# Optimization experiments

Hardware: AMD Instinct MI355X
Metric: run time of the kernel (lower is better)

Reference implementation:

```python
import jax, jax.numpy as jnp
import numpy as np

B, T, D = 2, 4096, 1024
H, HD = 16, 64
KV = H * HD  # 1024


def setup_inputs() -> dict:
    key = jax.random.key(0)
    ks = jax.random.split(key, 6)
    sc = lambda k, shape, s: jax.random.normal(k, shape, jnp.float32) * s
    return {
        "x": sc(ks[0], (B, T, D), 1.0),
        "W_in": sc(ks[1], (D, 4 * KV), D ** -0.5),      # in_proj (in, out) layout
        "W_ba": sc(ks[2], (D, 2 * H), D ** -0.5),       # ba_proj
        "conv_w": sc(ks[3], (3 * KV, 1, 4), 0.5),       # depthwise conv, (O, I/groups=1, K)
        "dt_bias": jnp.ones((H,), jnp.float32),
        "A_log": jnp.log(jax.random.uniform(ks[4], (H,), jnp.float32, 1e-3, 16.0)),
        "norm_w": jnp.ones((HD,), jnp.float32),
        "W_o": sc(ks[5], (KV, D), KV ** -0.5),
    }


def _l2norm(t, eps=1e-6):
    return t * jax.lax.rsqrt(jnp.sum(t * t, axis=-1, keepdims=True) + eps)


def reference(x, W_in, W_ba, conv_w, dt_bias, A_log, norm_w, W_o):
    Bb, Tt, _ = x.shape
    qkvz = x @ W_in                                  # [B,T,4*KV]
    q, k, v, z = jnp.split(qkvz, 4, axis=-1)
    b, a = jnp.split(x @ W_ba, 2, axis=-1)           # [B,T,H] each

    # causal depthwise conv (kernel 4, left pad 3) + SiLU on concat(q,k,v)
    qkv = jnp.concatenate([q, k, v], axis=-1).transpose(0, 2, 1)  # [B,3KV,T]
    qkv = jax.lax.conv_general_dilated(
        qkv, conv_w, window_strides=(1,), padding=[(3, 0)],
        feature_group_count=3 * KV, dimension_numbers=("NCH", "OIH", "NCH"))
    qkv = jax.nn.silu(qkv).transpose(0, 2, 1)        # [B,T,3KV]
    q, k, v = jnp.split(qkv, 3, axis=-1)

    rs = lambda t: t.reshape(Bb, Tt, H, HD)
    q, k, v, z = rs(q), rs(k), rs(v), rs(z)

    beta = jax.nn.sigmoid(b)                         # [B,T,H]
    A = jnp.exp(jnp.maximum(A_log, -2.3))            # [H]
    g = -A * jax.nn.softplus(a + dt_bias)            # [B,T,H], log decay <= 0

    # fla use_qk_l2norm_in_kernel=True: l2-normalize q,k; q scaled by d^-0.5
    q = _l2norm(q) * (HD ** -0.5)
    k = _l2norm(k)

    # gated delta rule recurrence over time (state S: [B,H,dk,dv])
    tm = lambda t: jnp.swapaxes(t, 0, 1)             # time-major

    def step(S, inp):
        qt, kt, vt, gt, bt = inp
        S = S * jnp.exp(gt)[..., None, None]
        pred = jnp.einsum("bhk,bhkv->bhv", kt, S)
        S = S + jnp.einsum("bhk,bhv->bhkv", kt, (vt - pred) * bt[..., None])
        o = jnp.einsum("bhk,bhkv->bhv", qt, S)
        return S, o

    S0 = jnp.zeros((Bb, H, HD, HD), jnp.float32)
    _, y = jax.lax.scan(step, S0, (tm(q), tm(k), tm(v), tm(g), tm(beta)))
    y = jnp.swapaxes(y, 0, 1)                        # [B,T,H,HD]

    # RMSNormGated over head_dim, gated by silu(z)
    y = y * jax.lax.rsqrt(jnp.mean(y * y, axis=-1, keepdims=True) + 1e-6)
    y = (norm_w * y) * jax.nn.silu(z)

    return y.reshape(Bb, Tt, KV) @ W_o
```

## Files before the change

kernel.cpp:

```cpp
#include <hip/hip_runtime.h>

typedef unsigned short u16;
typedef unsigned int u32;
typedef __attribute__((ext_vector_type(8))) __bf16 bf16x8;
typedef __attribute__((ext_vector_type(8))) _Float16 f16x8;
typedef __attribute__((ext_vector_type(4))) _Float16 f16x4;
typedef __attribute__((ext_vector_type(4))) float f32x4;

#define DEV __device__ __forceinline__

DEV u16 f2bf(float f) {
  u32 u = __float_as_uint(f);
  u += 0x7FFFu + ((u >> 16) & 1u);
  return (u16)(u >> 16);
}
DEV float bf2f(u16 h) { return __uint_as_float(((u32)h) << 16); }
DEV void splitbf(float f, u16& hi, u16& lo) {
  u16 h = f2bf(f);
  hi = h;
  lo = f2bf(f - bf2f(h));
}
DEV void split4(float4 v, ushort4& hh, ushort4& ll) {
  splitbf(v.x, hh.x, ll.x);
  splitbf(v.y, hh.y, ll.y);
  splitbf(v.z, hh.z, ll.z);
  splitbf(v.w, hh.w, ll.w);
}
DEV int SW(int r, int c) { return r * 64 + ((c) ^ ((r & 7) << 3)); }

#define MFMA16(a,b,c) __builtin_amdgcn_mfma_f32_16x16x32_bf16((a),(b),(c),0,0,0)
#define MFMAH(a,b,c)  __builtin_amdgcn_mfma_f32_16x16x32_f16((a),(b),(c),0,0,0)
#define GLDS16(g,l) __builtin_amdgcn_global_load_lds((__attribute__((address_space(1))) void*)(g), (__attribute__((address_space(3))) void*)(l), 16, 0, 0)

DEV f32x4 mm3(bf16x8 ah, bf16x8 al, bf16x8 bh, bf16x8 bl, f32x4 acc) {
  acc = MFMA16(ah, bl, acc);
  acc = MFMA16(al, bh, acc);
  acc = MFMA16(ah, bh, acc);
  return acc;
}

__global__ __launch_bounds__(256) void k_cast_h(const float* __restrict__ in, _Float16* __restrict__ out, int n) {
  int idx = (blockIdx.x * 256 + threadIdx.x) * 4;
  if (idx + 3 < n) {
    float4 v = *(const float4*)(in + idx);
    f16x4 o = {(_Float16)v.x, (_Float16)v.y, (_Float16)v.z, (_Float16)v.w};
    *(f16x4*)(out + idx) = o;
  }
}

__global__ __launch_bounds__(256) void k_transpose_h(const float* __restrict__ in, _Float16* __restrict__ out, int R, int Cc) {
  __shared__ float tile[64][65];
  int c0 = blockIdx.x * 64, r0 = blockIdx.y * 64;
  int lr = threadIdx.x >> 6, lc = threadIdx.x & 63;
#pragma unroll
  for (int i = 0; i < 16; ++i) {
    int r = lr + i * 4;
    tile[r][lc] = in[(size_t)(r0 + r) * Cc + c0 + lc];
  }
  __syncthreads();
#pragma unroll
  for (int i = 0; i < 16; ++i) {
    int oc = lr + i * 4;
    out[(size_t)(c0 + oc) * R + r0 + lc] = (_Float16)tile[lc][oc];
  }
}

__global__ __launch_bounds__(256) void k_transpose(const float* __restrict__ in, u16* __restrict__ out, int R, int Cc) {
  __shared__ float tile[64][65];
  int c0 = blockIdx.x * 64, r0 = blockIdx.y * 64;
  int lr = threadIdx.x >> 6, lc = threadIdx.x & 63;
#pragma unroll
  for (int i = 0; i < 16; ++i) {
    int r = lr + i * 4;
    tile[r][lc] = in[(size_t)(r0 + r) * Cc + c0 + lc];
  }
  __syncthreads();
#pragma unroll
  for (int i = 0; i < 16; ++i) {
    int oc = lr + i * 4;
    out[(size_t)(c0 + oc) * R + r0 + lc] = f2bf(tile[lc][oc]);
  }
}

__global__ __launch_bounds__(256) void k_gemm_h(const _Float16* __restrict__ A, const _Float16* __restrict__ Bt,
                                                u16* __restrict__ Cq, u16* __restrict__ Cz, int M, int N, int K) {
  __shared__ __align__(16) u16 As[128 * 32];
  __shared__ __align__(16) u16 Bs[128 * 32];
  const int tid = threadIdx.x;
  const int nwg = gridDim.x * gridDim.y;
  int bid = blockIdx.y * gridDim.x + blockIdx.x;
  bid = (bid & 7) * (nwg >> 3) + (bid >> 3);
  const int m0 = (bid / gridDim.x) * 128, n0 = (bid % gridDim.x) * 128;
  const int w = tid >> 6, l = tid & 63;
  const int wr = (w >> 1) * 64, wc = (w & 1) * 64;
  const int lrow = l & 15, lk = (l >> 4) * 8, rbase = (l >> 4) * 4;
  const int srow = tid >> 2, scol = (tid & 3) * 8;

  f32x4 acc[4][4];
#pragma unroll
  for (int i = 0; i < 4; ++i)
#pragma unroll
    for (int j = 0; j < 4; ++j) acc[i][j] = {0.f, 0.f, 0.f, 0.f};

  const _Float16* aBase = A + (size_t)m0 * K;
  const _Float16* bBase = Bt + (size_t)n0 * K;

  for (int k0 = 0; k0 < K; k0 += 32) {
    __syncthreads();
    GLDS16(aBase + (size_t)srow * K + k0 + scol,        &As[tid * 8]);
    GLDS16(aBase + (size_t)(srow + 64) * K + k0 + scol, &As[2048 + tid * 8]);
    GLDS16(bBase + (size_t)srow * K + k0 + scol,        &Bs[tid * 8]);
    GLDS16(bBase + (size_t)(srow + 64) * K + k0 + scol, &Bs[2048 + tid * 8]);
    __syncthreads();
    f16x8 af[4], bfr[4];
#pragma unroll
    for (int i = 0; i < 4; ++i) af[i] = *(const f16x8*)&As[(wr + i * 16 + lrow) * 32 + lk];
#pragma unroll
    for (int j = 0; j < 4; ++j) bfr[j] = *(const f16x8*)&Bs[(wc + j * 16 + lrow) * 32 + lk];
#pragma unroll
    for (int i = 0; i < 4; ++i)
#pragma unroll
      for (int j = 0; j < 4; ++j) acc[i][j] = MFMAH(af[i], bfr[j], acc[i][j]);
  }
#pragma unroll
  for (int i = 0; i < 4; ++i)
#pragma unroll
    for (int j = 0; j < 4; ++j)
#pragma unroll
      for (int r = 0; r < 4; ++r) {
        int row = m0 + wr + i * 16 + rbase + r;
        int col = n0 + wc + j * 16 + lrow;
        if (col < 3072) Cq[(size_t)row * 3072 + col] = f2bf(acc[i][j][r]);
        else            Cz[(size_t)row * 1024 + col - 3072] = f2bf(acc[i][j][r]);
      }
}

__global__ __launch_bounds__(256) void k_gemm2(const u16* __restrict__ Ah, const u16* __restrict__ Al,
                                               const u16* __restrict__ Bt, float* __restrict__ Cf,
                                               int M, int N, int K) {
  __shared__ __align__(16) u16 Ash[128 * 32];
  __shared__ __align__(16) u16 Asl[128 * 32];
  __shared__ __align__(16) u16 Bs[128 * 32];
  const int tid = threadIdx.x;
  const int nwg = gridDim.x * gridDim.y;
  int bid = blockIdx.y * gridDim.x + blockIdx.x;
  bid = (bid & 7) * (nwg >> 3) + (bid >> 3);
  const int m0 = (bid / gridDim.x) * 128, n0 = (bid % gridDim.x) * 128;
  const int w = tid >> 6, l = tid & 63;
  const int wr = (w >> 1) * 64, wc = (w & 1) * 64;
  const int lrow = l & 15, lk = (l >> 4) * 8, rbase = (l >> 4) * 4;
  const int srow = tid >> 2, scol = (tid & 3) * 8;

  f32x4 acc[4][4];
#pragma unroll
  for (int i = 0; i < 4; ++i)
#pragma unroll
    for (int j = 0; j < 4; ++j) acc[i][j] = {0.f, 0.f, 0.f, 0.f};

  const u16* ahBase = Ah + (size_t)m0 * K;
  const u16* alBase = Al + (size_t)m0 * K;
  const u16* bBase  = Bt + (size_t)n0 * K;

  for (int k0 = 0; k0 < K; k0 += 32) {
    __syncthreads();
    GLDS16(ahBase + (size_t)srow * K + k0 + scol,        &Ash[tid * 8]);
    GLDS16(ahBase + (size_t)(srow + 64) * K + k0 + scol, &Ash[2048 + tid * 8]);
    GLDS16(alBase + (size_t)srow * K + k0 + scol,        &Asl[tid * 8]);
    GLDS16(alBase + (size_t)(srow + 64) * K + k0 + scol, &Asl[2048 + tid * 8]);
    GLDS16(bBase + (size_t)srow * K + k0 + scol,         &Bs[tid * 8]);
    GLDS16(bBase + (size_t)(srow + 64) * K + k0 + scol,  &Bs[2048 + tid * 8]);
    __syncthreads();
    bf16x8 afh[4], afl[4], bfr[4];
#pragma unroll
    for (int i = 0; i < 4; ++i) afh[i] = *(const bf16x8*)&Ash[(wr + i * 16 + lrow) * 32 + lk];
#pragma unroll
    for (int i = 0; i < 4; ++i) afl[i] = *(const bf16x8*)&Asl[(wr + i * 16 + lrow) * 32 + lk];
#pragma unroll
    for (int j = 0; j < 4; ++j) bfr[j] = *(const bf16x8*)&Bs[(wc + j * 16 + lrow) * 32 + lk];
#pragma unroll
    for (int i = 0; i < 4; ++i)
#pragma unroll
      for (int j = 0; j < 4; ++j) {
        acc[i][j] = MFMA16(afl[i], bfr[j], acc[i][j]);
        acc[i][j] = MFMA16(afh[i], bfr[j], acc[i][j]);
      }
  }
#pragma unroll
  for (int i = 0; i < 4; ++i)
#pragma unroll
    for (int j = 0; j < 4; ++j)
#pragma unroll
      for (int r = 0; r < 4; ++r) {
        int row = m0 + wr + i * 16 + rbase + r;
        int col = n0 + wc + j * 16 + lrow;
        Cf[(size_t)row * N + col] = acc[i][j][r];
      }
}

__global__ __launch_bounds__(256) void k_ba(const float* __restrict__ x, const float* __restrict__ Wba,
                                            const float* __restrict__ dt_bias, const float* __restrict__ A_log,
                                            float* __restrict__ betaO, float* __restrict__ gO) {
  __shared__ float xs[4][1024];
  const int wid = threadIdx.x >> 6, lane = threadIdx.x & 63;
  const int m = blockIdx.x * 4 + wid;
#pragma unroll
  for (int i = 0; i < 16; ++i) xs[wid][lane + 64 * i] = x[(size_t)m * 1024 + lane + 64 * i];
  __syncthreads();
  const int n = lane & 31, half = lane >> 5;
  float acc = 0.f;
  const float* wp = Wba + n;
  const int kk0 = half * 512;
#pragma unroll 8
  for (int kk = kk0; kk < kk0 + 512; ++kk) acc += xs[wid][kk] * wp[kk * 32];
  acc += __shfl_xor(acc, 32);
  if (lane < 32) {
    if (n < 16) {
      betaO[(size_t)m * 16 + n] = 1.f / (1.f + expf(-acc));
    } else {
      int h = n - 16;
      float xx = acc + dt_bias[h];
      float sp = (xx > 20.f) ? xx : log1pf(expf(xx));
      gO[(size_t)m * 16 + h] = -expf(fmaxf(A_log[h], -2.3f)) * sp;
    }
  }
}

__global__ __launch_bounds__(256) void k_conv(const u16* __restrict__ qkv3, const float* __restrict__ convw,
                                              u16* __restrict__ qhG, u16* __restrict__ qlG,
                                              u16* __restrict__ khG, u16* __restrict__ klG,
                                              u16* __restrict__ vhG, u16* __restrict__ vlG) {
  __shared__ float cs[3072];
  __shared__ float innorm[32];
  const int bt = blockIdx.x;
  const int bb = bt >> 12, tt = bt & 4095;
  const int tid = threadIdx.x;
  const size_t rb = (size_t)bb * 4096;
#pragma unroll
  for (int s = 0; s < 3; ++s) {
    const int c4 = tid * 4 + s * 1024;
    float cwa[4][4];
#pragma unroll
    for (int e = 0; e < 4; ++e) {
      float4 t = *(const float4*)&convw[(c4 + e) * 4];
      cwa[e][0] = t.x; cwa[e][1] = t.y; cwa[e][2] = t.z; cwa[e][3] = t.w;
    }
    float acc[4] = {0.f, 0.f, 0.f, 0.f};
#pragma unroll
    for (int j = 0; j < 4; ++j) {
      const int tau = tt - 3 + j;
      if (tau >= 0) {
        ushort4 kv = *(const ushort4*)&qkv3[(rb + tau) * 3072 + c4];
        acc[0] += bf2f(kv.x) * cwa[0][j];
        acc[1] += bf2f(kv.y) * cwa[1][j];
        acc[2] += bf2f(kv.z) * cwa[2][j];
        acc[3] += bf2f(kv.w) * cwa[3][j];
      }
    }
#pragma unroll
    for (int e = 0; e < 4; ++e) cs[c4 + e] = acc[e] / (1.f + expf(-acc[e]));
  }
  __syncthreads();
  {
    const int grp = tid >> 3, off = (tid & 7) * 8;
    const float* p = cs + grp * 64 + off;
    float s = 0.f;
#pragma unroll
    for (int i = 0; i < 8; ++i) s += p[i] * p[i];
    s += __shfl_xor(s, 1); s += __shfl_xor(s, 2); s += __shfl_xor(s, 4);
    if ((tid & 7) == 0) innorm[grp] = rsqrtf(s + 1e-6f);
  }
  __syncthreads();
  const int h = tid >> 4, d4 = (tid & 15) * 4;
  const size_t ob = ((size_t)(bb * 16 + h) * 64 + (tt >> 6)) * 4096 + SW(tt & 63, d4);
  {
    const int ci = h * 64 + d4;
    const float sc = innorm[h] * 0.125f;
    float4 o = {cs[ci] * sc, cs[ci + 1] * sc, cs[ci + 2] * sc, cs[ci + 3] * sc};
    ushort4 hh, ll;
    split4(o, hh, ll);
    *(ushort4*)&qhG[ob] = hh;
    *(ushort4*)&qlG[ob] = ll;
  }
  {
    const int ci = 1024 + h * 64 + d4;
    const float sc = innorm[16 + h];
    float4 o = {cs[ci] * sc, cs[ci + 1] * sc, cs[ci + 2] * sc, cs[ci + 3] * sc};
    ushort4 hh, ll;
    split4(o, hh, ll);
    *(ushort4*)&khG[ob] = hh;
    *(ushort4*)&klG[ob] = ll;
  }
  {
    const int ci = 2048 + h * 64 + d4;
    float4 o = {cs[ci], cs[ci + 1], cs[ci + 2], cs[ci + 3]};
    ushort4 hh, ll;
    split4(o, hh, ll);
    *(ushort4*)&vhG[ob] = hh;
    *(ushort4*)&vlG[ob] = ll;
  }
}

__global__ __launch_bounds__(64) void k_prep(const u16* __restrict__ khG, const u16* __restrict__ klG,
                                             const float* __restrict__ gG, const float* __restrict__ betaG,
                                             float* __restrict__ gcG, u16* __restrict__ Tgh, u16* __restrict__ Tgl) {
  __shared__ __align__(16) char pmem[16384];
  u16* Kbh = (u16*)pmem;
  u16* Kbl = (u16*)(pmem + 8192);
  float* Af = (float*)pmem;
  __shared__ float gcs[64], bs[64];
  const int bhc = blockIdx.x;
  const int c = bhc & 63, h = (bhc >> 6) & 15, bb = bhc >> 10;
  const int lane = threadIdx.x;
  const int t0 = c * 64;
  const size_t rowbase = (size_t)bb * 4096;
  const size_t ktile = (size_t)bhc * 4096;
#pragma unroll
  for (int i = 0; i < 8; ++i) {
    const int idx = lane + 64 * i;
    GLDS16(khG + ktile + idx * 8, &Kbh[idx * 8]);
    GLDS16(klG + ktile + idx * 8, &Kbl[idx * 8]);
  }
  {
    float gv = gG[(rowbase + t0 + lane) * 16 + h];
    float sc = gv;
#pragma unroll
    for (int off = 1; off < 64; off <<= 1) {
      float o = __shfl_up(sc, off);
      if (lane >= off) sc += o;
    }
    gcs[lane] = sc;
    bs[lane] = betaG[(rowbase + t0 + lane) * 16 + h];
    gcG[(size_t)bhc * 64 + lane] = sc;
  }
  __syncthreads();
  const int lrow = lane & 15, lk8 = (lane >> 4) * 8, rbase = (lane >> 4) * 4;
  f32x4 acc[4][4];
#pragma unroll
  for (int i = 0; i < 4; ++i)
#pragma unroll
    for (int j = 0; j < 4; ++j) acc[i][j] = {0.f, 0.f, 0.f, 0.f};
#pragma unroll
  for (int ks = 0; ks < 2; ++ks) {
    bf16x8 afh[4], afl[4], bfh[4], bfl[4];
#pragma unroll
    for (int i = 0; i < 4; ++i) {
      afh[i] = *(const bf16x8*)&Kbh[SW(i * 16 + lrow, ks * 32 + lk8)];
      afl[i] = *(const bf16x8*)&Kbl[SW(i * 16 + lrow, ks * 32 + lk8)];
    }
#pragma unroll
    for (int j = 0; j < 4; ++j) {
      bfh[j] = *(const bf16x8*)&Kbh[SW(j * 16 + lrow, ks * 32 + lk8)];
      bfl[j] = *(const bf16x8*)&Kbl[SW(j * 16 + lrow, ks * 32 + lk8)];
    }
#pragma unroll
    for (int i = 0; i < 4; ++i)
#pragma unroll
      for (int j = 0; j < 4; ++j) acc[i][j] = mm3(afh[i], afl[i], bfh[j], bfl[j], acc[i][j]);
  }
  __syncthreads();
#pragma unroll
  for (int i = 0; i < 4; ++i)
#pragma unroll
    for (int j = 0; j < 4; ++j)
#pragma unroll
      for (int r = 0; r < 4; ++r) {
        int t = i * 16 + rbase + r, s = j * 16 + lrow;
        Af[t * 64 + s] = (s < t) ? bs[t] * expf(gcs[t] - gcs[s]) * acc[i][j][r] : 0.f;
      }
  __syncthreads();
  float x[64];
#pragma unroll
  for (int t = 0; t < 64; ++t) {
    float sum = 0.f;
#pragma unroll
    for (int s4 = 0; s4 + 4 <= t; s4 += 4) {
      float4 a4 = *(const float4*)&Af[t * 64 + s4];
      sum += a4.x * x[s4] + a4.y * x[s4 + 1] + a4.z * x[s4 + 2] + a4.w * x[s4 + 3];
    }
#pragma unroll
    for (int s = (t & ~3); s < t; ++s) sum += Af[t * 64 + s] * x[s];
    x[t] = ((t == lane) ? 1.f : 0.f) - sum;
  }
#pragma unroll
  for (int t = 0; t < 64; ++t) {
    u16 hi, lo;
    splitbf(x[t], hi, lo);
    Tgh[(size_t)bhc * 4096 + SW(t, lane)] = hi;
    Tgl[(size_t)bhc * 4096 + SW(t, lane)] = lo;
  }
}

__global__ __launch_bounds__(256) void k_mn(const u16* __restrict__ khG, const u16* __restrict__ klG,
                                            const u16* __restrict__ vhG, const u16* __restrict__ vlG,
                                            const u16* __restrict__ Tgh, const u16* __restrict__ Tgl,
                                            const float* __restrict__ gcG, const float* __restrict__ betaG,
                                            u16* __restrict__ Mh, u16* __restrict__ Ml,
                                            u16* __restrict__ Nh, u16* __restrict__ Nl) {
  extern __shared__ __align__(16) char smem[];
  u16* base = (u16*)smem;
  u16* Tbh  = base + 0 * 4096;
  u16* Tbl  = base + 1 * 4096;
  u16* X1h  = base + 2 * 4096;
  u16* X1l  = base + 3 * 4096;
  u16* KdTh = base + 4 * 4096;
  u16* KdTl = base + 5 * 4096;
  u16* X2h  = base + 6 * 4096;
  u16* X2l  = base + 7 * 4096;
  float* gcs = (float*)(base + 8 * 4096);
  float* bs  = gcs + 64;

  const int bhc = blockIdx.x;
  const int c = bhc & 63, h = (bhc >> 6) & 15, bb = bhc >> 10;
  const int tid = threadIdx.x, w = tid >> 6, l = tid & 63;
  const int lrow = l & 15, lk8 = (l >> 4) * 8, rbase = (l >> 4) * 4;
  const int t0 = c * 64;
  const size_t rowbase = (size_t)bb * 4096;
  const size_t ktile = (size_t)bhc * 4096;

  if (tid < 64) {
    gcs[tid] = gcG[(size_t)bhc * 64 + tid];
    bs[tid] = betaG[(rowbase + t0 + tid) * 16 + h];
  }
#pragma unroll
  for (int i = 0; i < 2; ++i) {
    const int idx = tid + 256 * i;
    const int off = idx * 8;
    *(float4*)&Tbh[off] = *(const float4*)&Tgh[(size_t)bhc * 4096 + off];
    *(float4*)&Tbl[off] = *(const float4*)&Tgl[(size_t)bhc * 4096 + off];
  }
  __syncthreads();
  const float gc63 = gcs[63];
#pragma unroll
  for (int i = 0; i < 16; ++i) {
    const int flat = tid + 256 * i;
    const int s = flat >> 6, d = flat & 63;
    const int sws = SW(s, d);
    const float kf = bf2f(khG[ktile + sws]) + bf2f(klG[ktile + sws]);
    const float gv = gcs[s], bv = bs[s];
    u16 hh, ll;
    splitbf(bv * expf(gv) * kf, hh, ll);
    X1h[SW(d, s)] = hh; X1l[SW(d, s)] = ll;
    splitbf(expf(gc63 - gv) * kf, hh, ll);
    KdTh[SW(d, s)] = hh; KdTl[SW(d, s)] = ll;
    const float vv = bf2f(vhG[ktile + sws]) + bf2f(vlG[ktile + sws]);
    splitbf(bv * vv, hh, ll);
    X2h[SW(d, s)] = hh; X2l[SW(d, s)] = ll;
  }
  __syncthreads();

  f32x4 aW[4], aU[4];
#pragma unroll
  for (int j = 0; j < 4; ++j) { aW[j] = {0.f,0.f,0.f,0.f}; aU[j] = {0.f,0.f,0.f,0.f}; }
#pragma unroll
  for (int ks = 0; ks < 2; ++ks) {
    const int ao = SW(w * 16 + lrow, ks * 32 + lk8);
    bf16x8 aTh = *(const bf16x8*)&Tbh[ao];
    bf16x8 aTl = *(const bf16x8*)&Tbl[ao];
#pragma unroll
    for (int j = 0; j < 4; ++j) {
      const int bo = SW(j * 16 + lrow, ks * 32 + lk8);
      aW[j] = mm3(aTh, aTl, *(const bf16x8*)&X1h[bo], *(const bf16x8*)&X1l[bo], aW[j]);
      aU[j] = mm3(aTh, aTl, *(const bf16x8*)&X2h[bo], *(const bf16x8*)&X2l[bo], aU[j]);
    }
  }
  __syncthreads();
#pragma unroll
  for (int j = 0; j < 4; ++j)
#pragma unroll
    for (int r = 0; r < 4; ++r) {
      const int t = w * 16 + rbase + r, dcol = j * 16 + lrow;
      u16 hh, ll;
      splitbf(aW[j][r], hh, ll);
      X1h[SW(dcol, t)] = hh; X1l[SW(dcol, t)] = ll;
      splitbf(aU[j][r], hh, ll);
      X2h[SW(dcol, t)] = hh; X2l[SW(dcol, t)] = ll;
    }
  __syncthreads();

  f32x4 aM[4], aN[4];
#pragma unroll
  for (int j = 0; j < 4; ++j) { aM[j] = {0.f,0.f,0.f,0.f}; aN[j] = {0.f,0.f,0.f,0.f}; }
#pragma unroll
  for (int ks = 0; ks < 2; ++ks) {
    const int ao = SW(w * 16 + lrow, ks * 32 + lk8);
    bf16x8 aKh = *(const bf16x8*)&KdTh[ao];
    bf16x8 aKl = *(const bf16x8*)&KdTl[ao];
#pragma unroll
    for (int j = 0; j < 4; ++j) {
      const int bo = SW(j * 16 + lrow, ks * 32 + lk8);
      aM[j] = mm3(aKh, aKl, *(const bf16x8*)&X1h[bo], *(const bf16x8*)&X1l[bo], aM[j]);
      aN[j] = mm3(aKh, aKl, *(const bf16x8*)&X2h[bo], *(const bf16x8*)&X2l[bo], aN[j]);
    }
  }
  __syncthreads();
  const float decC = expf(gc63);
#pragma unroll
  for (int j = 0; j < 4; ++j)
#pragma unroll
    for (int r = 0; r < 4; ++r) {
      const int d = w * 16 + rbase + r, d2 = j * 16 + lrow;
      u16 hh, ll;
      splitbf(((d == d2) ? decC : 0.f) - aM[j][r], hh, ll);
      X1h[SW(d, d2)] = hh; X1l[SW(d, d2)] = ll;
      splitbf(aN[j][r], hh, ll);
      X2h[SW(d, d2)] = hh; X2l[SW(d, d2)] = ll;
    }
  __syncthreads();
#pragma unroll
  for (int i = 0; i < 2; ++i) {
    const int idx = tid + 256 * i;
    const int off = idx * 8;
    *(float4*)&Mh[(size_t)bhc * 4096 + off] = *(const float4*)&X1h[off];
    *(float4*)&Ml[(size_t)bhc * 4096 + off] = *(const float4*)&X1l[off];
    *(float4*)&Nh[(size_t)bhc * 4096 + off] = *(const float4*)&X2h[off];
    *(float4*)&Nl[(size_t)bhc * 4096 + off] = *(const float4*)&X2l[off];
  }
}

__global__ __launch_bounds__(256) void k_seg(const u16* __restrict__ Mh, const u16* __restrict__ Ml,
                                             const u16* __restrict__ Nh, const u16* __restrict__ Nl,
                                             u16* __restrict__ Msegh, u16* __restrict__ Msegl,
                                             u16* __restrict__ Nsegh, u16* __restrict__ Nsegl) {
  extern __shared__ __align__(16) char smem[];
  u16* base = (u16*)smem;
  u16* MaTh = base + 0 * 4096;
  u16* MaTl = base + 1 * 4096;
  u16* NaTh = base + 2 * 4096;
  u16* NaTl = base + 3 * 4096;
  u16* sMh  = base + 4 * 4096;
  u16* sMl  = base + 5 * 4096;
  u16* sNh  = base + 6 * 4096;
  u16* sNl  = base + 7 * 4096;

  const int blk = blockIdx.x;
  const size_t cbase = (size_t)(blk >> 3) * 64 + (blk & 7) * 8;
  const int tid = threadIdx.x, w = tid >> 6, l = tid & 63;
  const int lrow = l & 15, lk8 = (l >> 4) * 8, rbase = (l >> 4) * 4;

#pragma unroll
  for (int i = 0; i < 2; ++i) {
    const int off = (tid + 256 * i) * 8;
    *(float4*)&sMh[off] = *(const float4*)&Mh[cbase * 4096 + off];
    *(float4*)&sMl[off] = *(const float4*)&Ml[cbase * 4096 + off];
    *(float4*)&sNh[off] = *(const float4*)&Nh[cbase * 4096 + off];
    *(float4*)&sNl[off] = *(const float4*)&Nl[cbase * 4096 + off];
  }
  __syncthreads();
#pragma unroll
  for (int i = 0; i < 16; ++i) {
    const int flat = tid + 256 * i;
    const int a = flat >> 6, b = flat & 63;
    MaTh[SW(a, b)] = sMh[SW(b, a)];
    MaTl[SW(a, b)] = sMl[SW(b, a)];
    NaTh[SW(a, b)] = sNh[SW(b, a)];
    NaTl[SW(a, b)] = sNl[SW(b, a)];
  }
  __syncthreads();

  for (int j = 1; j < 8; ++j) {
#pragma unroll
    for (int i = 0; i < 2; ++i) {
      const int off = (tid + 256 * i) * 8;
      *(float4*)&sMh[off] = *(const float4*)&Mh[(cbase + j) * 4096 + off];
      *(float4*)&sMl[off] = *(const float4*)&Ml[(cbase + j) * 4096 + off];
      *(float4*)&sNh[off] = *(const float4*)&Nh[(cbase + j) * 4096 + off];
      *(float4*)&sNl[off] = *(const float4*)&Nl[(cbase + j) * 4096 + off];
    }
    __syncthreads();
    f32x4 aM2[4], aN2[4];
#pragma unroll
    for (int jj = 0; jj < 4; ++jj) { aM2[jj] = {0.f,0.f,0.f,0.f}; aN2[jj] = {0.f,0.f,0.f,0.f}; }
#pragma unroll
    for (int ks = 0; ks < 2; ++ks) {
      const int ao = SW(w * 16 + lrow, ks * 32 + lk8);
      bf16x8 aCh = *(const bf16x8*)&sMh[ao];
      bf16x8 aCl = *(const bf16x8*)&sMl[ao];
#pragma unroll
      for (int jj = 0; jj < 4; ++jj) {
        const int bo = SW(jj * 16 + lrow, ks * 32 + lk8);
        aM2[jj] = mm3(aCh, aCl, *(const bf16x8*)&MaTh[bo], *(const bf16x8*)&MaTl[bo], aM2[jj]);
        aN2[jj] = mm3(aCh, aCl, *(const bf16x8*)&NaTh[bo], *(const bf16x8*)&NaTl[bo], aN2[jj]);
      }
    }
    __syncthreads();
#pragma unroll
    for (int jj = 0; jj < 4; ++jj)
#pragma unroll
      for (int r = 0; r < 4; ++r) {
        const int t = w * 16 + rbase + r, col = jj * 16 + lrow;
        u16 hh, ll;
        splitbf(aM2[jj][r], hh, ll);
        MaTh[SW(col, t)] = hh; MaTl[SW(col, t)] = ll;
        const float nv = aN2[jj][r] + bf2f(sNh[SW(t, col)]) + bf2f(sNl[SW(t, col)]);
        splitbf(nv, hh, ll);
        NaTh[SW(col, t)] = hh; NaTl[SW(col, t)] = ll;
      }
    __syncthreads();
  }
#pragma unroll
  for (int i = 0; i < 16; ++i) {
    const int flat = tid + 256 * i;
    const int t = flat >> 6, s = flat & 63;
    Msegh[(size_t)blk * 4096 + SW(t, s)] = MaTh[SW(s, t)];
    Msegl[(size_t)blk * 4096 + SW(t, s)] = MaTl[SW(s, t)];
    Nsegh[(size_t)blk * 4096 + SW(t, s)] = NaTh[SW(s, t)];
    Nsegl[(size_t)blk * 4096 + SW(t, s)] = NaTl[SW(s, t)];
  }
}

__global__ __launch_bounds__(256) void k_bound(const u16* __restrict__ Msegh, const u16* __restrict__ Msegl,
                                               const u16* __restrict__ Nsegh, const u16* __restrict__ Nsegl,
                                               u16* __restrict__ Ssegh, u16* __restrict__ Ssegl) {
  __shared__ __align__(16) u16 STh[4096], STl[4096];
  __shared__ __align__(16) u16 sMh[4096], sMl[4096], sNh[4096], sNl[4096];
  const int bh = blockIdx.x;
  const int tid = threadIdx.x, w = tid >> 6, l = tid & 63;
  const int lrow = l & 15, lk8 = (l >> 4) * 8, rbase = (l >> 4) * 4;
  for (int i = tid; i < 4096; i += 256) { STh[i] = (u16)0; STl[i] = (u16)0; }
  __syncthreads();
  for (int j = 0; j < 8; ++j) {
    const size_t sb = (size_t)(bh * 8 + j) * 4096;
#pragma unroll
    for (int i = 0; i < 2; ++i) {
      const int off = (tid + 256 * i) * 8;
      *(float4*)&Ssegh[sb + off] = *(const float4*)&STh[off];
      *(float4*)&Ssegl[sb + off] = *(const float4*)&STl[off];
      *(float4*)&sMh[off] = *(const float4*)&Msegh[sb + off];
      *(float4*)&sMl[off] = *(const float4*)&Msegl[sb + off];
      *(float4*)&sNh[off] = *(const float4*)&Nsegh[sb + off];
      *(float4*)&sNl[off] = *(const float4*)&Nsegl[sb + off];
    }
    __syncthreads();
    f32x4 acc[4];
#pragma unroll
    for (int jj = 0; jj < 4; ++jj) acc[jj] = {0.f, 0.f, 0.f, 0.f};
#pragma unroll
    for (int ks = 0; ks < 2; ++ks) {
      const int ao = SW(w * 16 + lrow, ks * 32 + lk8);
      bf16x8 aSh = *(const bf16x8*)&STh[ao];
      bf16x8 aSl = *(const bf16x8*)&STl[ao];
#pragma unroll
      for (int jj = 0; jj < 4; ++jj) {
        const int bo = SW(jj * 16 + lrow, ks * 32 + lk8);
        acc[jj] = mm3(aSh, aSl, *(const bf16x8*)&sMh[bo], *(const bf16x8*)&sMl[bo], acc[jj]);
      }
    }
    __syncthreads();
#pragma unroll
    for (int jj = 0; jj < 4; ++jj)
#pragma unroll
      for (int r = 0; r < 4; ++r) {
        const int v = w * 16 + rbase + r, t = jj * 16 + lrow;
        const float sv = acc[jj][r] + bf2f(sNh[SW(t, v)]) + bf2f(sNl[SW(t, v)]);
        u16 hh, ll;
        splitbf(sv, hh, ll);
        STh[SW(v, t)] = hh; STl[SW(v, t)] = ll;
      }
    __syncthreads();
  }
}

__global__ __launch_bounds__(512, 2) void k_scan2(const u16* __restrict__ qhG, const u16* __restrict__ qlG,
                                               const u16* __restrict__ khG, const u16* __restrict__ klG,
                                               const u16* __restrict__ vhG, const u16* __restrict__ vlG,
                                               const u16* __restrict__ zb,
                                               const u16* __restrict__ Tgh, const u16* __restrict__ Tgl,
                                               const float* __restrict__ gcG,
                                               const float* __restrict__ betaG, const float* __restrict__ norm_w,
                                               const u16* __restrict__ Ssegh, const u16* __restrict__ Ssegl,
                                               u16* __restrict__ Yhi, u16* __restrict__ Ylo) {
  extern __shared__ __align__(16) char smem[];
  u16* base = (u16*)smem;
  u16* Kbh  = base + 0 * 4096;
  u16* Kbl  = base + 1 * 4096;
  u16* Qbh  = base + 2 * 4096;
  u16* Qbl  = base + 3 * 4096;
  u16* Vbh  = base + 4 * 4096;
  u16* Vbl  = base + 5 * 4096;
  u16* Zb   = base + 6 * 4096;
  u16* Tbh  = base + 7 * 4096;
  u16* Tbl  = base + 8 * 4096;
  u16* SbTh = base + 9 * 4096;
  u16* SbTl = base + 10 * 4096;
  u16* Mqh  = base + 11 * 4096;
  u16* Mql  = base + 12 * 4096;
  u16* KdTh = base + 13 * 4096;
  u16* KdTl = base + 14 * 4096;
  u16* RTh  = base + 15 * 4096;
  u16* RTl  = base + 16 * 4096;
  u16* UTh  = base + 17 * 4096;
  u16* UTl  = base + 18 * 4096;
  u16* Ybh  = RTh;
  u16* Ybl  = RTl;
  float* gcs = (float*)(base + 19 * 4096);
  float* bs  = gcs + 64;
  float* nws = gcs + 128;
  float* esF = gcs + 192;
  float* etF = gcs + 256;
  float* ssP = gcs + 320;

  const int blk = blockIdx.x;
  const int bh = blk >> 3, seg = blk & 7;
  const int bb = bh >> 4, h = bh & 15;
  const int tid = threadIdx.x, w = tid >> 6, l = tid & 63;
  const int wrow = w >> 1, jh = w & 1;
  const int lrow = l & 15, lk8 = (l >> 4) * 8, rbase = (l >> 4) * 4;
  const size_t rowbase = (size_t)bb * 4096;
  const size_t bhTile = (size_t)bh * 64;
  const int o8 = tid * 8;
  const int zr = tid >> 3, zc8 = (tid & 7) << 3;

  {
    const int c = seg * 8, t0 = c * 64;
    const size_t gt = (bhTile + c) * 4096;
    GLDS16(qhG + gt + o8, &Qbh[o8]);
    GLDS16(qlG + gt + o8, &Qbl[o8]);
    GLDS16(khG + gt + o8, &Kbh[o8]);
    GLDS16(klG + gt + o8, &Kbl[o8]);
    GLDS16(vhG + gt + o8, &Vbh[o8]);
    GLDS16(vlG + gt + o8, &Vbl[o8]);
    GLDS16(Tgh + (size_t)(bh * 64 + c) * 4096 + o8, &Tbh[o8]);
    GLDS16(Tgl + (size_t)(bh * 64 + c) * 4096 + o8, &Tbl[o8]);
    GLDS16(Ssegh + (size_t)blk * 4096 + o8, &SbTh[o8]);
    GLDS16(Ssegl + (size_t)blk * 4096 + o8, &SbTl[o8]);
    *(float4*)&Zb[SW(zr, zc8)] = *(const float4*)&zb[(rowbase + t0 + zr) * 1024 + h * 64 + zc8];
    if (tid < 64) {
      nws[tid] = norm_w[tid];
      float g0 = gcG[((size_t)bh * 64 + c) * 64 + tid];
      float b0 = betaG[(rowbase + t0 + tid) * 16 + h];
      float g63 = __shfl(g0, 63);
      gcs[tid] = g0; bs[tid] = b0;
      esF[tid] = expf(g63 - g0);
      etF[tid] = expf(g0);
    }
  }
  __syncthreads();

  for (int cc = 0; cc < 8; ++cc) {
    const int c = seg * 8 + cc;
    const int t0 = c * 64;
    const bool pf = (cc < 7);
    const size_t gt1 = (bhTile + c + 1) * 4096;

    float4 pz;
    float pgc = 0.f, pbs = 0.f;
    if (pf) {
      const int t1 = t0 + 64;
      pz = *(const float4*)&zb[(rowbase + t1 + zr) * 1024 + h * 64 + zc8];
      if (tid < 64) {
        pgc = gcG[((size_t)bh * 64 + (c + 1)) * 64 + tid];
        pbs = betaG[(rowbase + t1 + tid) * 16 + h];
      }
    }

#pragma unroll
    for (int i = 0; i < 8; ++i) {
      const int flat = tid * 8 + i;
      const int d = flat >> 6, s = flat & 63;
      const float kv = bf2f(Kbh[SW(s, d)]) + bf2f(Kbl[SW(s, d)]);
      u16 hh, ll;
      splitbf(esF[s] * kv, hh, ll);
      KdTh[SW(d, s)] = hh;
      KdTl[SW(d, s)] = ll;
    }
    f32x4 aqk[2], ap[2], aqs[2];
#pragma unroll
    for (int j = 0; j < 2; ++j) { aqk[j] = {0.f,0.f,0.f,0.f}; ap[j] = {0.f,0.f,0.f,0.f}; aqs[j] = {0.f,0.f,0.f,0.f}; }
#pragma unroll
    for (int ks = 0; ks < 2; ++ks) {
      const int ao = SW(wrow * 16 + lrow, ks * 32 + lk8);
      bf16x8 aKh = *(const bf16x8*)&Kbh[ao];
      bf16x8 aKl = *(const bf16x8*)&Kbl[ao];
      bf16x8 aQh = *(const bf16x8*)&Qbh[ao];
      bf16x8 aQl = *(const bf16x8*)&Qbl[ao];
#pragma unroll
      for (int j = 0; j < 2; ++j) {
        const int jj = jh * 2 + j;
        const int bo = SW(jj * 16 + lrow, ks * 32 + lk8);
        bf16x8 bKh = *(const bf16x8*)&Kbh[bo];
        bf16x8 bKl = *(const bf16x8*)&Kbl[bo];
        bf16x8 bSh = *(const bf16x8*)&SbTh[bo];
        bf16x8 bSl = *(const bf16x8*)&SbTl[bo];
        aqk[j] = mm3(aQh, aQl, bKh, bKl, aqk[j]);
        ap[j]  = mm3(aKh, aKl, bSh, bSl, ap[j]);
        aqs[j] = mm3(aQh, aQl, bSh, bSl, aqs[j]);
      }
    }
#pragma unroll
    for (int j = 0; j < 2; ++j)
#pragma unroll
      for (int r = 0; r < 4; ++r) {
        const int t = wrow * 16 + rbase + r;
        const int s = (jh * 2 + j) * 16 + lrow;
        u16 mh, ml;
        splitbf((s <= t) ? expf(gcs[t] - gcs[s]) * aqk[j][r] : 0.f, mh, ml);
        Mqh[SW(t, s)] = mh;
        Mql[SW(t, s)] = ml;
        const float vv = bf2f(Vbh[SW(t, s)]) + bf2f(Vbl[SW(t, s)]);
        const float rhs = bs[t] * (vv - etF[t] * ap[j][r]);
        u16 rh, rl;
        splitbf(rhs, rh, rl);
        RTh[SW(s, t)] = rh;
        RTl[SW(s, t)] = rl;
      }
    __syncthreads();

    if (pf) {
      GLDS16(qhG + gt1 + o8, &Qbh[o8]);
      GLDS16(qlG + gt1 + o8, &Qbl[o8]);
      GLDS16(khG + gt1 + o8, &Kbh[o8]);
      GLDS16(klG + gt1 + o8, &Kbl[o8]);
      GLDS16(vhG + gt1 + o8, &Vbh[o8]);
      GLDS16(vlG + gt1 + o8, &Vbl[o8]);
    }

    f32x4 au[2];
#pragma unroll
    for (int j = 0; j < 2; ++j) au[j] = {0.f, 0.f, 0.f, 0.f};
#pragma unroll
    for (int ks = 0; ks < 2; ++ks) {
      const int ao = SW(wrow * 16 + lrow, ks * 32 + lk8);
      bf16x8 aTh = *(const bf16x8*)&Tbh[ao];
      bf16x8 aTl = *(const bf16x8*)&Tbl[ao];
#pragma unroll
      for (int j = 0; j < 2; ++j) {
        const int bo = SW((jh * 2 + j) * 16 + lrow, ks * 32 + lk8);
        au[j] = mm3(aTh, aTl, *(const bf16x8*)&RTh[bo], *(const bf16x8*)&RTl[bo], au[j]);
      }
    }
#pragma unroll
    for (int j = 0; j < 2; ++j)
#pragma unroll
      for (int r = 0; r < 4; ++r) {
        u16 uh, ul;
        splitbf(au[j][r], uh, ul);
        const int o = SW((jh * 2 + j) * 16 + lrow, wrow * 16 + rbase + r);
        UTh[o] = uh;
        UTl[o] = ul;
      }
    __syncthreads();

    if (pf) {
      GLDS16(Tgh + (size_t)(bh * 64 + (c + 1)) * 4096 + o8, &Tbh[o8]);
      GLDS16(Tgl + (size_t)(bh * 64 + (c + 1)) * 4096 + o8, &Tbl[o8]);
    }

    f32x4 amu[2], as_[2];
#pragma unroll
    for (int j = 0; j < 2; ++j) { amu[j] = {0.f,0.f,0.f,0.f}; as_[j] = {0.f,0.f,0.f,0.f}; }
#pragma unroll
    for (int ks = 0; ks < 2; ++ks) {
      const int ao = SW(wrow * 16 + lrow, ks * 32 + lk8);
      bf16x8 aMh = *(const bf16x8*)&Mqh[ao];
      bf16x8 aMl = *(const bf16x8*)&Mql[ao];
      bf16x8 aKdh = *(const bf16x8*)&KdTh[ao];
      bf16x8 aKdl = *(const bf16x8*)&KdTl[ao];
#pragma unroll
      for (int j = 0; j < 2; ++j) {
        const int bo = SW((jh * 2 + j) * 16 + lrow, ks * 32 + lk8);
        bf16x8 bUh = *(const bf16x8*)&UTh[bo];
        bf16x8 bUl = *(const bf16x8*)&UTl[bo];
        amu[j] = mm3(aMh, aMl, bUh, bUl, amu[j]);
        as_[j] = mm3(aKdh, aKdl, bUh, bUl, as_[j]);
      }
    }
    float yv_[4][2];
#pragma unroll
    for (int r = 0; r < 4; ++r) {
      const int t = wrow * 16 + rbase + r;
      const float gt = etF[t];
      float ss = 0.f;
#pragma unroll
      for (int j = 0; j < 2; ++j) {
        yv_[r][j] = gt * aqs[j][r] + amu[j][r];
        ss += yv_[r][j] * yv_[r][j];
      }
      ss += __shfl_xor(ss, 1); ss += __shfl_xor(ss, 2); ss += __shfl_xor(ss, 4); ss += __shfl_xor(ss, 8);
      if (lrow == 0) ssP[jh * 64 + t] = ss;
    }
    __syncthreads();
#pragma unroll
    for (int r = 0; r < 4; ++r) {
      const int t = wrow * 16 + rbase + r;
      const float rstd = rsqrtf((ssP[t] + ssP[64 + t]) * (1.f / 64.f) + 1e-6f);
#pragma unroll
      for (int j = 0; j < 2; ++j) {
        const int col = (jh * 2 + j) * 16 + lrow;
        const float zz = bf2f(Zb[SW(t, col)]);
        const float yv = yv_[r][j] * rstd * nws[col] * (zz / (1.f + expf(-zz)));
        u16 yh, yl;
        splitbf(yv, yh, yl);
        Ybh[SW(t, col)] = yh;
        Ybl[SW(t, col)] = yl;
      }
    }
    {
      const float decC = etF[63];
#pragma unroll
      for (int j = 0; j < 2; ++j)
#pragma unroll
        for (int r = 0; r < 4; ++r) {
          const int d = wrow * 16 + rbase + r, col = (jh * 2 + j) * 16 + lrow;
          const int o = SW(col, d);
          const float s0 = bf2f(SbTh[o]) + bf2f(SbTl[o]);
          const float sv = decC * s0 + as_[j][r];
          u16 sh, sl;
          splitbf(sv, sh, sl);
          SbTh[o] = sh;
          SbTl[o] = sl;
        }
    }
    __syncthreads();

    {
      const size_t grow = (rowbase + t0 + zr) * 1024 + h * 64 + zc8;
      *(float4*)&Yhi[grow] = *(const float4*)&Ybh[SW(zr, zc8)];
      *(float4*)&Ylo[grow] = *(const float4*)&Ybl[SW(zr, zc8)];
    }
    if (pf) {
      *(float4*)&Zb[SW(zr, zc8)] = pz;
      if (tid < 64) {
        float g63 = __shfl(pgc, 63);
        gcs[tid] = pgc; bs[tid] = pbs;
        esF[tid] = expf(g63 - pgc);
        etF[tid] = expf(pgc);
      }
    }
    __syncthreads();
  }
}

extern "C" void kernel_launch(void* const* d_in, const int* in_sizes, int n_in,
                              void* d_out, int out_size, void* d_ws, size_t ws_size,
                              hipStream_t stream) {
  (void)in_sizes; (void)n_in; (void)out_size; (void)ws_size;
  const float* x       = (const float*)d_in[0];
  const float* W_in    = (const float*)d_in[1];
  const float* W_ba    = (const float*)d_in[2];
  const float* conv_w  = (const float*)d_in[3];
  const float* dt_bias = (const float*)d_in[4];
  const float* A_log   = (const float*)d_in[5];
  const float* norm_w  = (const float*)d_in[6];
  const float* W_o     = (const float*)d_in[7];
  float* out = (float*)d_out;
  char* ws = (char*)d_ws;
  const size_t MB = 1048576;

  _Float16* xh = (_Float16*)(ws + 0);
  u16* MhB   = (u16*)(ws + 0);
  u16* YhiB  = (u16*)(ws + 0);
  u16* MlB   = (u16*)(ws + 16 * MB);
  u16* YloB  = (u16*)(ws + 16 * MB);
  _Float16* WinT = (_Float16*)(ws + 32 * MB);
  float* gB  = (float*)(ws + 32 * MB);
  float* bB  = (float*)(ws + 32 * MB + 524288);
  float* gcB = (float*)(ws + 33 * MB);
  u16* Ssegh = (u16*)(ws + 34 * MB);
  u16* Ssegl = (u16*)(ws + 36 * MB);
  u16* Msegh = (u16*)(ws + 38 * MB);
  u16* Msegl = (u16*)(ws + 40 * MB);
  u16* Nsegh = (u16*)(ws + 42 * MB);
  u16* Nsegl = (u16*)(ws + 44 * MB);
  u16* WoT   = (u16*)(ws + 48 * MB);
  u16* qkv3  = (u16*)(ws + 50 * MB);
  u16* NhB   = (u16*)(ws + 50 * MB);
  u16* NlB   = (u16*)(ws + 66 * MB);
  u16* zbB   = (u16*)(ws + 98 * MB);
  u16* qhG   = (u16*)(ws + 114 * MB);
  u16* qlG   = (u16*)(ws + 130 * MB);
  u16* khG   = (u16*)(ws + 146 * MB);
  u16* klG   = (u16*)(ws + 162 * MB);
  u16* vhG   = (u16*)(ws + 178 * MB);
  u16* vlG   = (u16*)(ws + 194 * MB);
  u16* TghB  = (u16*)(ws + 210 * MB);
  u16* TglB  = (u16*)(ws + 226 * MB);

  const int SCAN_LDS = 19 * 8192 + 448 * 4;
  const int MN_LDS   = 8 * 8192 + 512;
  const int SEG_LDS  = 8 * 8192;

  k_cast_h<<<8192, 256, 0, stream>>>(x, xh, 8388608);
  k_transpose_h<<<dim3(64, 16), 256, 0, stream>>>(W_in, WinT, 1024, 4096);
  k_transpose<<<dim3(16, 16), 256, 0, stream>>>(W_o, WoT, 1024, 1024);
  k_gemm_h<<<dim3(32, 64), 256, 0, stream>>>(xh, WinT, qkv3, zbB, 8192, 4096, 1024);
  k_ba<<<2048, 256, 0, stream>>>(x, W_ba, dt_bias, A_log, bB, gB);
  k_conv<<<8192, 256, 0, stream>>>(qkv3, conv_w, qhG, qlG, khG, klG, vhG, vlG);
  k_prep<<<2048, 64, 0, stream>>>(khG, klG, gB, bB, gcB, TghB, TglB);
  hipFuncSetAttribute((const void*)k_mn, hipFuncAttributeMaxDynamicSharedMemorySize, MN_LDS);
  k_mn<<<2048, 256, MN_LDS, stream>>>(khG, klG, vhG, vlG, TghB, TglB, gcB, bB, MhB, MlB, NhB, NlB);
  hipFuncSetAttribute((const void*)k_seg, hipFuncAttributeMaxDynamicSharedMemorySize, SEG_LDS);
  k_seg<<<256, 256, SEG_LDS, stream>>>(MhB, MlB, NhB, NlB, Msegh, Msegl, Nsegh, Nsegl);
  k_bound<<<32, 256, 0, stream>>>(Msegh, Msegl, Nsegh, Nsegl, Ssegh, Ssegl);
  hipFuncSetAttribute((const void*)k_scan2, hipFuncAttributeMaxDynamicSharedMemorySize, SCAN_LDS);
  k_scan2<<<256, 512, SCAN_LDS, stream>>>(qhG, qlG, khG, klG, vhG, vlG, zbB, TghB, TglB, gcB, bB, norm_w,
                                          Ssegh, Ssegl, YhiB, YloB);
  k_gemm2<<<dim3(8, 64), 256, 0, stream>>>(YhiB, YloB, WoT, out, 8192, 1024, 1024);
}
```

Before: 528.7 us.

## Pre-swizzle GEMM operands in global memory to avoid LDS bank conflicts

Producers of the GEMM operands (cast, transposes, and the recurrence's Y output) now write rows in a permuted layout. Because global_load_lds copies 16-byte chunks straight into LDS, the chunks land in an XOR-swizzled arrangement. The GEMM fragment reads then use a matching swizzled index, aiming to remove LDS bank conflicts on the MFMA operand loads. The risk is that every producer and consumer must agree exactly on the permutation, and the transpose stores become slightly less regular.

New measurement: 528.6 us. No clear change (-0.0%).

```diff
diff --git a/kernel.cpp b/kernel.cpp
--- a/kernel.cpp
+++ b/kernel.cpp
@@ -28,6 +28,20 @@
 }
 DEV int SW(int r, int c) { return r * 64 + ((c) ^ ((r & 7) << 3)); }
 
+DEV int SWG(int r, int c) {
+  int db = ((r & 1) << 2) | ((c >> 3) & 3);
+  int dbp = db ^ ((r >> 1) & 7);
+  return ((r >> 1) << 6) | (dbp << 3) | (c & 7);
+}
+DEV size_t gidx_swz(size_t row, int col, int rowlen) {
+  int rr7 = (int)((row >> 1) & 7);
+  int db = (int)(((row & 1) << 2) | ((col >> 3) & 3));
+  int dbp = db ^ rr7;
+  size_t rowp = (row & ~(size_t)1) | (size_t)(dbp >> 2);
+  int colp = (col & ~31) | ((dbp & 3) << 3) | (col & 7);
+  return rowp * (size_t)rowlen + colp;
+}
+
 #define MFMA16(a,b,c) __builtin_amdgcn_mfma_f32_16x16x32_bf16((a),(b),(c),0,0,0)
 #define MFMAH(a,b,c)  __builtin_amdgcn_mfma_f32_16x16x32_f16((a),(b),(c),0,0,0)
 #define GLDS16(g,l) __builtin_amdgcn_global_load_lds((__attribute__((address_space(1))) void*)(g), (__attribute__((address_space(3))) void*)(l), 16, 0, 0)
@@ -44,7 +58,9 @@
   if (idx + 3 < n) {
     float4 v = *(const float4*)(in + idx);
     f16x4 o = {(_Float16)v.x, (_Float16)v.y, (_Float16)v.z, (_Float16)v.w};
-    *(f16x4*)(out + idx) = o;
+    const size_t row = (size_t)(idx >> 10);
+    const int col = idx & 1023;
+    *(f16x4*)(out + gidx_swz(row, col, 1024)) = o;
   }
 }
 
@@ -61,7 +77,7 @@
 #pragma unroll
   for (int i = 0; i < 16; ++i) {
     int oc = lr + i * 4;
-    out[(size_t)(c0 + oc) * R + r0 + lc] = (_Float16)tile[lc][oc];
+    out[gidx_swz((size_t)(c0 + oc), r0 + lc, R)] = (_Float16)tile[lc][oc];
   }
 }
 
@@ -78,7 +94,7 @@
 #pragma unroll
   for (int i = 0; i < 16; ++i) {
     int oc = lr + i * 4;
-    out[(size_t)(c0 + oc) * R + r0 + lc] = f2bf(tile[lc][oc]);
+    out[gidx_swz((size_t)(c0 + oc), r0 + lc, R)] = f2bf(tile[lc][oc]);
   }
 }
 
@@ -114,9 +130,9 @@
     __syncthreads();
     f16x8 af[4], bfr[4];
 #pragma unroll
-    for (int i = 0; i < 4; ++i) af[i] = *(const f16x8*)&As[(wr + i * 16 + lrow) * 32 + lk];
-#pragma unroll
-    for (int j = 0; j < 4; ++j) bfr[j] = *(const f16x8*)&Bs[(wc + j * 16 + lrow) * 32 + lk];
+    for (int i = 0; i < 4; ++i) af[i] = *(const f16x8*)&As[SWG(wr + i * 16 + lrow, lk)];
+#pragma unroll
+    for (int j = 0; j < 4; ++j) bfr[j] = *(const f16x8*)&Bs[SWG(wc + j * 16 + lrow, lk)];
 #pragma unroll
     for (int i = 0; i < 4; ++i)
 #pragma unroll
@@ -172,11 +188,11 @@
     __syncthreads();
     bf16x8 afh[4], afl[4], bfr[4];
 #pragma unroll
-    for (int i = 0; i < 4; ++i) afh[i] = *(const bf16x8*)&Ash[(wr + i * 16 + lrow) * 32 + lk];
-#pragma unroll
-    for (int i = 0; i < 4; ++i) afl[i] = *(const bf16x8*)&Asl[(wr + i * 16 + lrow) * 32 + lk];
-#pragma unroll
-    for (int j = 0; j < 4; ++j) bfr[j] = *(const bf16x8*)&Bs[(wc + j * 16 + lrow) * 32 + lk];
+    for (int i = 0; i < 4; ++i) afh[i] = *(const bf16x8*)&Ash[SWG(wr + i * 16 + lrow, lk)];
+#pragma unroll
+    for (int i = 0; i < 4; ++i) afl[i] = *(const bf16x8*)&Asl[SWG(wr + i * 16 + lrow, lk)];
+#pragma unroll
+    for (int j = 0; j < 4; ++j) bfr[j] = *(const bf16x8*)&Bs[SWG(wc + j * 16 + lrow, lk)];
 #pragma unroll
     for (int i = 0; i < 4; ++i)
 #pragma unroll
@@ -913,9 +929,9 @@
     __syncthreads();
 
     {
-      const size_t grow = (rowbase + t0 + zr) * 1024 + h * 64 + zc8;
-      *(float4*)&Yhi[grow] = *(const float4*)&Ybh[SW(zr, zc8)];
-      *(float4*)&Ylo[grow] = *(const float4*)&Ybl[SW(zr, zc8)];
+      const size_t gsw = gidx_swz(rowbase + t0 + zr, h * 64 + zc8, 1024);
+      *(float4*)&Yhi[gsw] = *(const float4*)&Ybh[SW(zr, zc8)];
+      *(float4*)&Ylo[gsw] = *(const float4*)&Ybl[SW(zr, zc8)];
     }
     if (pf) {
       *(float4*)&Zb[SW(zr, zc8)] = pz;
```
